# Kernel tuning notes

Measured on AMD Instinct MI355X. Metric: run time of the kernel, lower is better.

Reference implementation:

```python
import jax, jax.numpy as jnp
import numpy as np

M, A, H, T = 6, 4096, 128, 30   # num_modes, num_actors, hidden_size, future_steps
HIST = 50
MAX_T = 6.0
DT = MAX_T / T                   # min_stepsize: one Euler step per prediction interval
MIN_SCALE = 0.001
EPS = 1e-5

def _ln(x, g, b):
    mu = x.mean(-1, keepdims=True)
    v = ((x - mu) ** 2).mean(-1, keepdims=True)
    return (x - mu) * jax.lax.rsqrt(v + EPS) * g + b

def setup_inputs() -> dict:
    key = jax.random.key(0)
    ks = iter(jax.random.split(key, 64))
    def p(shape):
        return jax.random.normal(next(ks), shape, jnp.float32) * 0.02
    inp = {
        'local_embed':  jax.random.normal(next(ks), (A, H), jnp.float32),
        'global_embed': jax.random.normal(next(ks), (M, A, H), jnp.float32),
        'noise':        jax.random.normal(next(ks), (T, M * A, H), jnp.float32),
        # aggr_embed: Linear(2H,H) + LayerNorm
        'aggr_w': p((2 * H, H)), 'aggr_b': p((H,)),
        'aggr_g': jnp.ones((H,), jnp.float32), 'aggr_be': jnp.zeros((H,), jnp.float32),
        # FFunc (posterior drift): Linear(H+2,H)-Tanh-Linear(H,H)-Tanh-Linear(H,H)
        'f_w1': p((H + 2, H)), 'f_b1': p((H,)),
        'f_w2': p((H, H)),     'f_b2': p((H,)),
        'f_w3': p((H, H)),     'f_b3': p((H,)),
        # GFunc (diffusion): Linear(H+2,H)-Tanh-Linear(H,H)-Tanh-Linear(H,1)-Sigmoid
        'g_w1': p((H + 2, H)), 'g_b1': p((H,)),
        'g_w2': p((H, H)),     'g_b2': p((H,)),
        'g_w3': p((H, 1)),     'g_b3': p((1,)),
        # decoder: Linear(H,H)+LN+ReLU+Linear(H,2)
        'd_w1': p((H, H)), 'd_b1': p((H,)),
        'd_g': jnp.ones((H,), jnp.float32), 'd_be': jnp.zeros((H,), jnp.float32),
        'd_w2': p((H, 2)), 'd_b2': p((2,)),
        # scale head (uncertain=True): same structure as decoder
        's_w1': p((H, H)), 's_b1': p((H,)),
        's_g': jnp.ones((H,), jnp.float32), 's_be': jnp.zeros((H,), jnp.float32),
        's_w2': p((H, 2)), 's_b2': p((2,)),
        # pi head: Linear(2H,H)+LN+ReLU+Linear(H,1)
        'p_w1': p((2 * H, H)), 'p_b1': p((H,)),
        'p_g': jnp.ones((H,), jnp.float32), 'p_be': jnp.zeros((H,), jnp.float32),
        'p_w2': p((H, 1)), 'p_b2': p((1,)),
        'padding_mask': jnp.zeros((A, HIST), dtype=bool),
    }
    return inp

def reference(local_embed, global_embed, noise,
              aggr_w, aggr_b, aggr_g, aggr_be,
              f_w1, f_b1, f_w2, f_b2, f_w3, f_b3,
              g_w1, g_b1, g_w2, g_b2, g_w3, g_b3,
              d_w1, d_b1, d_g, d_be, d_w2, d_b2,
              s_w1, s_b1, s_g, s_be, s_w2, s_b2,
              p_w1, p_b1, p_g, p_be, p_w2, p_b2,
              padding_mask):
    N = M * A
    le = jnp.broadcast_to(local_embed, (M, A, H))
    # aggr_embed(cat(global, local))
    x = jnp.concatenate([global_embed, le], axis=-1)
    h0 = jax.nn.relu(_ln(x @ aggr_w + aggr_b, aggr_g, aggr_be)).reshape(N, H)

    def with_time(y, t):
        tc = jnp.ones((y.shape[0], 1), y.dtype) * t
        return jnp.concatenate([y, jnp.sin(tc), jnp.cos(tc)], axis=-1)

    def drift(t, y):  # FFunc
        i = with_time(y, t)
        h = jnp.tanh(i @ f_w1 + f_b1)
        h = jnp.tanh(h @ f_w2 + f_b2)
        return h @ f_w3 + f_b3

    def diffusion(t, y):  # GFunc -> scalar per sample, repeated over dims
        i = with_time(y, t)
        h = jnp.tanh(i @ g_w1 + g_b1)
        h = jnp.tanh(h @ g_w2 + g_b2)
        return jax.nn.sigmoid(h @ g_w3 + g_b3)  # [N,1]

    ts = jnp.linspace(0.0, MAX_T, T + 1)[:-1]  # left endpoints of each Euler step
    sqdt = jnp.sqrt(jnp.asarray(DT, h0.dtype))

    def step(y, tz):
        t, z = tz
        y2 = y + drift(t, y) * DT + diffusion(t, y) * sqdt * z
        return y2, y2

    _, ys = jax.lax.scan(step, h0, (ts, noise))  # [T, N, H]
    sol_y = ys.transpose(1, 0, 2)                # [N, T, H]

    dh = jax.nn.relu(_ln(sol_y @ d_w1 + d_b1, d_g, d_be))
    loc = (dh @ d_w2 + d_b2).reshape(M, A, T, 2)
    sh = jax.nn.relu(_ln(sol_y @ s_w1 + s_b1, s_g, s_be))
    scale = jax.nn.elu(sh @ s_w2 + s_b2) + 1.0 + MIN_SCALE
    scale = scale.reshape(M, A, T, 2)
    loc_out = jnp.concatenate([loc, scale], axis=-1)  # [M, A, T, 4]

    pin = jnp.concatenate([le, global_embed], axis=-1)
    pi = (jax.nn.relu(_ln(pin @ p_w1 + p_b1, p_g, p_be)) @ p_w2 + p_b2)
    pi = pi.squeeze(-1).T                              # [A, M]

    reg_mask = ~padding_mask[:, -T:]
    return loc_out, pi, reg_mask
```

## Files before the change

kernel.cpp:

```cpp
#include <hip/hip_runtime.h>

#define Adim 4096
#define HD 128
#define TSTEPS 30
#define NROWS 24576
#define RBLK 32
#define NBLKS 768
#define DT_C 0.2f
#define SQDT_C 0.44721359549995794f
#define LN_EPS 1e-5f

#define PI_OFF   2949120
#define MASK_OFF 2973696

typedef unsigned short u16;
typedef __bf16 bf16x8 __attribute__((ext_vector_type(8)));
typedef float f32x4 __attribute__((ext_vector_type(4)));

__device__ __forceinline__ u16 f2bf(float x){
    unsigned u = __builtin_bit_cast(unsigned, x);
    u = (u + 0x7fffu + ((u >> 16) & 1u)) >> 16;
    return (u16)u;
}
__device__ __forceinline__ float bf2f(unsigned h){
    unsigned u = (h & 0xffffu) << 16;
    return __builtin_bit_cast(float, u);
}
__device__ __forceinline__ unsigned pack2(float a, float b){
    unsigned r;
    asm("v_cvt_pk_bf16_f32 %0, %1, %2" : "=v"(r) : "v"(a), "v"(b));
    return r;
}
__device__ __forceinline__ float tanh_f(float x){
    return 1.0f - 2.0f / (1.0f + __expf(2.0f * x));
}
__device__ __forceinline__ float sigm_f(float x){
    return 1.0f / (1.0f + __expf(-x));
}
#define SWZ(r,k) ((k) ^ (((r)&7)<<3))

#define MFMA(A,B,C) __builtin_amdgcn_mfma_f32_16x16x32_bf16(A, B, C, 0, 0, 0)

__device__ __forceinline__ void loadW(const u16* __restrict__ img, int lane, int wid,
                                      bf16x8 W[4]) {
    const int c = wid*16 + (lane & 15);
    const int kq = lane >> 4;
#pragma unroll
    for (int kk = 0; kk < 4; ++kk)
        W[kk] = *reinterpret_cast<const bf16x8*>(img + c*HD + SWZ(c, kk*32 + kq*8));
}

__device__ __forceinline__ void gemm1(const u16* __restrict__ act, const bf16x8 (&W)[4],
                                      int lane, f32x4 acc[2]) {
    const int rl = lane & 15, kq = lane >> 4;
#pragma unroll
    for (int tr = 0; tr < 2; ++tr) {
        const int r = tr*16 + rl;
        const u16* arow = act + r*HD;
        f32x4 a = {0.f,0.f,0.f,0.f};
#pragma unroll
        for (int kk = 0; kk < 4; ++kk) {
            bf16x8 bf = *reinterpret_cast<const bf16x8*>(arow + SWZ(r, kk*32 + kq*8));
            a = MFMA(W[kk], bf, a);
        }
        acc[tr] = a;
    }
}
__device__ __forceinline__ void gemm2(const u16* __restrict__ act,
                                      const bf16x8 (&Wx)[4], const bf16x8 (&Wy)[4],
                                      int lane, f32x4 accX[2], f32x4 accY[2]) {
    const int rl = lane & 15, kq = lane >> 4;
#pragma unroll
    for (int tr = 0; tr < 2; ++tr) {
        const int r = tr*16 + rl;
        const u16* arow = act + r*HD;
        f32x4 ax = {0.f,0.f,0.f,0.f}, ay = {0.f,0.f,0.f,0.f};
#pragma unroll
        for (int kk = 0; kk < 4; ++kk) {
            bf16x8 bf = *reinterpret_cast<const bf16x8*>(arow + SWZ(r, kk*32 + kq*8));
            ax = MFMA(Wx[kk], bf, ax);
            ay = MFMA(Wy[kk], bf, ay);
        }
        accX[tr] = ax; accY[tr] = ay;
    }
}
__device__ __forceinline__ void gemm4(const u16* __restrict__ act,
                                      const bf16x8 (&W1)[4], const bf16x8 (&W2)[4],
                                      const bf16x8 (&W3)[4], const bf16x8 (&W4)[4],
                                      int lane, f32x4 a1[2], f32x4 a2[2],
                                      f32x4 a3[2], f32x4 a4[2]) {
    const int rl = lane & 15, kq = lane >> 4;
#pragma unroll
    for (int tr = 0; tr < 2; ++tr) {
        const int r = tr*16 + rl;
        const u16* arow = act + r*HD;
        f32x4 x1={0.f,0.f,0.f,0.f}, x2={0.f,0.f,0.f,0.f};
        f32x4 x3={0.f,0.f,0.f,0.f}, x4={0.f,0.f,0.f,0.f};
#pragma unroll
        for (int kk = 0; kk < 4; ++kk) {
            bf16x8 bf = *reinterpret_cast<const bf16x8*>(arow + SWZ(r, kk*32 + kq*8));
            x1 = MFMA(W1[kk], bf, x1);
            x2 = MFMA(W2[kk], bf, x2);
            x3 = MFMA(W3[kk], bf, x3);
            x4 = MFMA(W4[kk], bf, x4);
        }
        a1[tr]=x1; a2[tr]=x2; a3[tr]=x3; a4[tr]=x4;
    }
}

__device__ __forceinline__ void epiT(const f32x4 acc[2], const float b[4],
                                     u16* dst, int lane, int wid) {
    const int c0 = wid*16 + ((lane>>4)<<2);
    const int rl = lane & 15;
#pragma unroll
    for (int tr = 0; tr < 2; ++tr) {
        int r = tr*16 + rl;
        float v0 = tanh_f(acc[tr][0] + b[0]);
        float v1 = tanh_f(acc[tr][1] + b[1]);
        float v2 = tanh_f(acc[tr][2] + b[2]);
        float v3 = tanh_f(acc[tr][3] + b[3]);
        uint2 pk = { pack2(v0, v1), pack2(v2, v3) };
        *reinterpret_cast<uint2*>(dst + r*HD + SWZ(r, c0)) = pk;
    }
}
__device__ __forceinline__ void epiN(const f32x4 acc[2], const float b[4],
                                     u16* dst, int lane, int wid) {
    const int c0 = wid*16 + ((lane>>4)<<2);
    const int rl = lane & 15;
#pragma unroll
    for (int tr = 0; tr < 2; ++tr) {
        int r = tr*16 + rl;
        uint2 pk = { pack2(acc[tr][0]+b[0], acc[tr][1]+b[1]),
                     pack2(acc[tr][2]+b[2], acc[tr][3]+b[3]) };
        *reinterpret_cast<uint2*>(dst + r*HD + SWZ(r, c0)) = pk;
    }
}
__device__ __forceinline__ void epiF(const f32x4 acc[2], const float* __restrict__ bias,
                                     float* dst, int lane, int wid) {
    const int c0 = wid*16 + ((lane>>4)<<2);
    const int rl = lane & 15;
    float4 b4 = *reinterpret_cast<const float4*>(bias + c0);
#pragma unroll
    for (int tr = 0; tr < 2; ++tr) {
        int r = tr*16 + rl;
        float4 v = { acc[tr][0]+b4.x, acc[tr][1]+b4.y, acc[tr][2]+b4.z, acc[tr][3]+b4.w };
        *reinterpret_cast<float4*>(dst + r*HD + c0) = v;
    }
}

__device__ __forceinline__ void gemmX(const u16* __restrict__ Xc, int kBase,
                                      const u16* __restrict__ img,
                                      int lane, int wid, f32x4 acc[2], bool init) {
    bf16x8 W[4]; loadW(img, lane, wid, W);
    const int rl = lane & 15, kq = lane >> 4;
#pragma unroll
    for (int tr = 0; tr < 2; ++tr) {
        const int r = tr*16 + rl;
        const u16* arow = Xc + r*256;
        f32x4 a = init ? f32x4{0.f,0.f,0.f,0.f} : acc[tr];
#pragma unroll
        for (int kk = 0; kk < 4; ++kk) {
            bf16x8 bf = *reinterpret_cast<const bf16x8*>(arow + SWZ(r, kBase + kk*32 + kq*8));
            a = MFMA(W[kk], bf, a);
        }
        acc[tr] = a;
    }
}

__device__ __forceinline__ void head_ln(const u16* __restrict__ src,
                                        const float4* __restrict__ pp4,
                                        float b20, float b21, int elu, int off, int idx,
                                        float* __restrict__ outStage)
{
    int row = idx >> 3, sub = idx & 7;
    int c0 = sub * 16;
    uint4 p0 = *reinterpret_cast<const uint4*>(src + row*HD + SWZ(row, c0));
    uint4 p1 = *reinterpret_cast<const uint4*>(src + row*HD + SWZ(row, c0+8));
    float v[16];
    v[0]=bf2f(p0.x); v[1]=bf2f(p0.x>>16); v[2]=bf2f(p0.y); v[3]=bf2f(p0.y>>16);
    v[4]=bf2f(p0.z); v[5]=bf2f(p0.z>>16); v[6]=bf2f(p0.w); v[7]=bf2f(p0.w>>16);
    v[8]=bf2f(p1.x); v[9]=bf2f(p1.x>>16); v[10]=bf2f(p1.y); v[11]=bf2f(p1.y>>16);
    v[12]=bf2f(p1.z); v[13]=bf2f(p1.z>>16); v[14]=bf2f(p1.w); v[15]=bf2f(p1.w>>16);
    float s = 0.f, sq = 0.f;
#pragma unroll
    for (int i = 0; i < 16; ++i){ s += v[i]; sq += v[i]*v[i]; }
    s += __shfl_xor(s,1); sq += __shfl_xor(sq,1);
    s += __shfl_xor(s,2); sq += __shfl_xor(sq,2);
    s += __shfl_xor(s,4); sq += __shfl_xor(sq,4);
    float mu = s * (1.f/128.f);
    float rstd = rsqrtf(sq*(1.f/128.f) - mu*mu + LN_EPS);
    float a0 = 0.f, a1 = 0.f;
#pragma unroll
    for (int i = 0; i < 16; ++i){
        float4 p = pp4[(c0 + i) ^ sub];
        float h = (v[i]-mu)*rstd*p.x + p.y;
        h = fmaxf(h, 0.f);
        a0 += h * p.z; a1 += h * p.w;
    }
    a0 += __shfl_xor(a0,1); a1 += __shfl_xor(a1,1);
    a0 += __shfl_xor(a0,2); a1 += __shfl_xor(a1,2);
    a0 += __shfl_xor(a0,4); a1 += __shfl_xor(a1,4);
    if (sub == 0){
        a0 += b20; a1 += b21;
        if (elu){
            a0 = (a0 > 0.f ? a0 : __expf(a0)-1.f) + 1.001f;
            a1 = (a1 > 0.f ? a1 : __expf(a1)-1.f) + 1.001f;
        }
        outStage[row*4 + off]   = a0;
        outStage[row*4 + off+1] = a1;
    }
}

__global__ void prep_w(const float* __restrict__ fw1, const float* __restrict__ fw2,
                       const float* __restrict__ fw3, const float* __restrict__ gw1,
                       const float* __restrict__ gw2, const float* __restrict__ dw1,
                       const float* __restrict__ sw1, const float* __restrict__ aw,
                       const float* __restrict__ pw1, u16* __restrict__ ws)
{
    int img = blockIdx.y;
    int idx = blockIdx.x * 256 + threadIdx.x;
    int k = idx >> 7, j = idx & 127;
    const float* W = fw1; int sr = k;
    switch (img) {
        case 0: W = fw1; break;  case 1: W = fw2; break;  case 2: W = fw3; break;
        case 3: W = gw1; break;  case 4: W = gw2; break;
        case 5: W = dw1; break;  case 6: W = sw1; break;
        case 7: W = aw;  break;  case 8: W = aw;  sr = k + 128; break;
        case 9: W = pw1; break;  case 10: W = pw1; sr = k + 128; break;
    }
    ws[(size_t)img*16384 + j*128 + SWZ(j, k)] = f2bf(W[(size_t)sr*128 + j]);
}

__global__ void reorder_out(const float* __restrict__ wsOut, float* __restrict__ outp)
{
    __shared__ float tile[3840];
    int b = blockIdx.x;
    const float* src = wsOut + (size_t)b*3840;
#pragma unroll
    for (int j = 0; j < 15; ++j) {
        int idx = j*256 + threadIdx.x;
        int tt = idx >> 7, rc = idx & 127;
        int row = rc >> 2, c = idx & 3;
        tile[row*120 + tt*4 + c] = src[idx];
    }
    __syncthreads();
    float* dst = outp + (size_t)b*3840;
#pragma unroll
    for (int j = 0; j < 15; ++j) {
        int idx = j*256 + threadIdx.x;
        dst[idx] = tile[idx];
    }
}

__global__ __launch_bounds__(512, 2) void sde_fused(
    const float* __restrict__ lE, const float* __restrict__ gE,
    const float* __restrict__ noise,
    const float* __restrict__ aggr_b, const float* __restrict__ aggr_g, const float* __restrict__ aggr_be,
    const float* __restrict__ fw1, const float* __restrict__ fb1,
    const float* __restrict__ fb2, const float* __restrict__ fb3,
    const float* __restrict__ gw1, const float* __restrict__ gb1,
    const float* __restrict__ gb2, const float* __restrict__ gw3, const float* __restrict__ gb3,
    const float* __restrict__ db1, const float* __restrict__ dg, const float* __restrict__ dbe,
    const float* __restrict__ dw2, const float* __restrict__ db2,
    const float* __restrict__ sb1, const float* __restrict__ sg, const float* __restrict__ sbe,
    const float* __restrict__ sw2, const float* __restrict__ sb2,
    const float* __restrict__ pb1, const float* __restrict__ pg, const float* __restrict__ pbe,
    const float* __restrict__ pw2, const float* __restrict__ pb2,
    const unsigned char* __restrict__ pmask,
    const u16* __restrict__ wimg,
    float* __restrict__ wsOut,
    float* __restrict__ outp)
{
    __shared__ __align__(16) unsigned char SMEM[61952];
    u16*  Sb    = (u16*)SMEM;
    u16*  Ab    = (u16*)(SMEM + 8192);
    u16*  Bb    = (u16*)(SMEM + 16384);
    u16*  Cb    = (u16*)(SMEM + 24576);
    u16*  Fb    = (u16*)(SMEM + 32768);
    u16*  Db    = (u16*)(SMEM + 40960);
    u16*  Eb    = (u16*)(SMEM + 49152);
    float4* ppd = (float4*)(SMEM + 57344);
    float4* pps = (float4*)(SMEM + 59392);
    float* outStage = (float*)(SMEM + 61440);
    u16*  Xc    = (u16*)(SMEM + 40960);
    float* preLN = (float*)(SMEM + 8192);

    const int tid  = threadIdx.x;
    const int lane = tid & 63;
    const int wid  = tid >> 6;
    const int bid  = blockIdx.x;
    const int r0   = bid * RBLK;
    const int c0e  = wid*16 + ((lane>>4)<<2);

    if (tid < 128) {
        int cs = tid ^ ((tid >> 4) & 7);
        ppd[cs] = make_float4(dg[tid], dbe[tid], dw2[2*tid], dw2[2*tid+1]);
        pps[cs] = make_float4(sg[tid], sbe[tid], sw2[2*tid], sw2[2*tid+1]);
    }
#pragma unroll
    for (int i = 0; i < 2; ++i) {
        int gidx = i*512 + tid;
        int r = gidx >> 5;
        int k = (gidx & 31) * 8;
        int gr = r0 + r;
        const float* src = (k < HD) ? (gE + (size_t)gr*HD + k)
                                    : (lE + (size_t)(gr & (Adim-1))*HD + (k - HD));
        float4 v0 = reinterpret_cast<const float4*>(src)[0];
        float4 v1 = reinterpret_cast<const float4*>(src)[1];
        uint4 pk = { pack2(v0.x, v0.y), pack2(v0.z, v0.w),
                     pack2(v1.x, v1.y), pack2(v1.z, v1.w) };
        *reinterpret_cast<uint4*>(Xc + r*256 + SWZ(r, k)) = pk;
    }
    __syncthreads();

    f32x4 acc[2];

    gemmX(Xc, 0,   wimg + 10*16384, lane, wid, acc, true);
    gemmX(Xc, 128, wimg + 9*16384,  lane, wid, acc, false);
    epiF(acc, pb1, preLN, lane, wid);
    __syncthreads();
    {
        int row = tid >> 4, sub = tid & 15;
        int c0 = sub * 8;
        const float* yr = preLN + row*HD + c0;
        float v[8]; float s = 0.f, sq = 0.f;
#pragma unroll
        for (int i = 0; i < 8; ++i){ float x = yr[i]; v[i] = x; s += x; sq += x*x; }
        s += __shfl_xor(s,1); sq += __shfl_xor(sq,1);
        s += __shfl_xor(s,2); sq += __shfl_xor(sq,2);
        s += __shfl_xor(s,4); sq += __shfl_xor(sq,4);
        s += __shfl_xor(s,8); sq += __shfl_xor(sq,8);
        float mu = s*(1.f/128.f);
        float rstd = rsqrtf(sq*(1.f/128.f) - mu*mu + LN_EPS);
        float a0 = 0.f;
#pragma unroll
        for (int i = 0; i < 8; ++i){
            int cc = c0 + i;
            float h = (v[i]-mu)*rstd*pg[cc] + pbe[cc];
            a0 += fmaxf(h, 0.f) * pw2[cc];
        }
        a0 += __shfl_xor(a0,1); a0 += __shfl_xor(a0,2);
        a0 += __shfl_xor(a0,4); a0 += __shfl_xor(a0,8);
        if (sub == 0) {
            int gr = r0 + row;
            outp[PI_OFF + (size_t)(gr & (Adim-1))*6 + (gr >> 12)] = a0 + pb2[0];
        }
    }
    if (tid < RBLK) {
        int gr = r0 + tid;
        if (gr < Adim) {
            const unsigned char* pm = pmask + (size_t)gr*50 + 20;
            float* o = outp + MASK_OFF + (size_t)gr*TSTEPS;
#pragma unroll
            for (int i = 0; i < TSTEPS; ++i) o[i] = pm[i] ? 0.f : 1.f;
        }
    }
    __syncthreads();

    gemmX(Xc, 0,   wimg + 7*16384, lane, wid, acc, true);
    gemmX(Xc, 128, wimg + 8*16384, lane, wid, acc, false);
    __syncthreads();
    epiF(acc, aggr_b, preLN, lane, wid);
    __syncthreads();

    float y0,y1,y2,y3,y4,y5,y6,y7;
    {
        int row = tid >> 4, sub = tid & 15;
        int c0 = sub * 8;
        const float* yr = preLN + row*HD + c0;
        float v[8]; float s = 0.f, sq = 0.f;
#pragma unroll
        for (int i = 0; i < 8; ++i){ float x = yr[i]; v[i] = x; s += x; sq += x*x; }
        s += __shfl_xor(s,1); sq += __shfl_xor(sq,1);
        s += __shfl_xor(s,2); sq += __shfl_xor(sq,2);
        s += __shfl_xor(s,4); sq += __shfl_xor(sq,4);
        s += __shfl_xor(s,8); sq += __shfl_xor(sq,8);
        float mu = s*(1.f/128.f);
        float rstd = rsqrtf(sq*(1.f/128.f) - mu*mu + LN_EPS);
#pragma unroll
        for (int i = 0; i < 8; ++i){
            int cc = c0 + i;
            float h = (v[i]-mu)*rstd*aggr_g[cc] + aggr_be[cc];
            v[i] = fmaxf(h, 0.f);
        }
        y0=v[0]; y1=v[1]; y2=v[2]; y3=v[3]; y4=v[4]; y5=v[5]; y6=v[6]; y7=v[7];
        uint4 pk = { pack2(v[0],v[1]), pack2(v[2],v[3]),
                     pack2(v[4],v[5]), pack2(v[6],v[7]) };
        *reinterpret_cast<uint4*>(&Sb[row*HD + SWZ(row, c0)]) = pk;
    }

    bf16x8 WF1[4], WG1[4], WF2[4], WG2[4], WF3[4], WD1[4], WS1[4];
    loadW(wimg + 0*16384, lane, wid, WF1);
    loadW(wimg + 3*16384, lane, wid, WG1);
    loadW(wimg + 1*16384, lane, wid, WF2);
    loadW(wimg + 4*16384, lane, wid, WG2);
    loadW(wimg + 2*16384, lane, wid, WF3);
    loadW(wimg + 5*16384, lane, wid, WD1);
    loadW(wimg + 6*16384, lane, wid, WS1);

    float fb2c[4], gb2c[4], fb3c[4], db1c[4], sb1c[4];
    float fb1c[4], gb1c[4], fw1s[4], fw1cc[4], gw1s[4], gw1cc[4];
#pragma unroll
    for (int q = 0; q < 4; ++q) {
        int c = c0e + q;
        fb2c[q]=fb2[c]; gb2c[q]=gb2[c]; fb3c[q]=fb3[c]; db1c[q]=db1[c]; sb1c[q]=sb1[c];
        fb1c[q]=fb1[c]; gb1c[q]=gb1[c];
        fw1s[q]=fw1[128*HD+c]; fw1cc[q]=fw1[129*HD+c];
        gw1s[q]=gw1[128*HD+c]; gw1cc[q]=gw1[129*HD+c];
    }
    float g3r[8];
#pragma unroll
    for (int j = 0; j < 8; ++j) g3r[j] = gw3[(tid & 15)*8 + j];
    const float db20 = db2[0], db21 = db2[1];
    const float sb20 = sb2[0], sb21 = sb2[1];
    const float gb3v = gb3[0];

    float4 nz0, nz1;
    __syncthreads();

    {
        float bF[4], bG[4];
#pragma unroll
        for (int q = 0; q < 4; ++q) { bF[q] = fb1c[q] + fw1cc[q]; bG[q] = gb1c[q] + gw1cc[q]; }
        f32x4 aF[2], aG[2];
        gemm2(Sb, WF1, WG1, lane, aF, aG);
        epiT(aF, bF, Ab, lane, wid);
        epiT(aG, bG, Bb, lane, wid);
        const float* np = noise + ((size_t)r0)*HD + (size_t)tid*8;
        nz0 = reinterpret_cast<const float4*>(np)[0];
        nz1 = reinterpret_cast<const float4*>(np)[1];
    }
    __syncthreads();

    for (int k = 0; k < TSTEPS; ++k) {
        {
            f32x4 a1[2];
            gemm1(Ab, WF2, lane, a1);
            epiT(a1, fb2c, Cb, lane, wid);
            gemm1(Bb, WG2, lane, a1);
            epiT(a1, gb2c, Fb, lane, wid);
        }
        if (k) {
            if (tid < 256) head_ln(Db, ppd, db20, db21, 0, 0, tid, outStage);
            else           head_ln(Eb, pps, sb20, sb21, 1, 2, tid-256, outStage);
        }
        __syncthreads();
        {
            f32x4 a1[2];
            gemm1(Cb, WF3, lane, a1);
            epiN(a1, fb3c, Db, lane, wid);
        }
        float growv;
        {
            int row = tid >> 4, sub = tid & 15;
            uint4 pk = *reinterpret_cast<const uint4*>(Fb + row*HD + SWZ(row, sub*8));
            float s = bf2f(pk.x)*g3r[0] + bf2f(pk.x>>16)*g3r[1]
                    + bf2f(pk.y)*g3r[2] + bf2f(pk.y>>16)*g3r[3]
                    + bf2f(pk.z)*g3r[4] + bf2f(pk.z>>16)*g3r[5]
                    + bf2f(pk.w)*g3r[6] + bf2f(pk.w>>16)*g3r[7];
            s += __shfl_xor(s,1); s += __shfl_xor(s,2);
            s += __shfl_xor(s,4); s += __shfl_xor(s,8);
            growv = sigm_f(s + gb3v);
        }
        __syncthreads();
        {
            int row = tid >> 4, sub = tid & 15;
            int sk = SWZ(row, sub*8);
            uint4 dpk = *reinterpret_cast<const uint4*>(Db + row*HD + sk);
            float g = growv * SQDT_C;
            y0 += bf2f(dpk.x)     * DT_C + g*nz0.x;
            y1 += bf2f(dpk.x>>16) * DT_C + g*nz0.y;
            y2 += bf2f(dpk.y)     * DT_C + g*nz0.z;
            y3 += bf2f(dpk.y>>16) * DT_C + g*nz0.w;
            y4 += bf2f(dpk.z)     * DT_C + g*nz1.x;
            y5 += bf2f(dpk.z>>16) * DT_C + g*nz1.y;
            y6 += bf2f(dpk.w)     * DT_C + g*nz1.z;
            y7 += bf2f(dpk.w>>16) * DT_C + g*nz1.w;
            uint4 s4 = { pack2(y0,y1), pack2(y2,y3), pack2(y4,y5), pack2(y6,y7) };
            *reinterpret_cast<uint4*>(Sb + row*HD + sk) = s4;
        }
        __syncthreads();
        if (k < TSTEPS-1) {
            float t = (k+1) * DT_C;
            float st = __sinf(t), ct = __cosf(t);
            float bF[4], bG[4];
#pragma unroll
            for (int q = 0; q < 4; ++q) {
                bF[q] = fb1c[q] + st*fw1s[q] + ct*fw1cc[q];
                bG[q] = gb1c[q] + st*gw1s[q] + ct*gw1cc[q];
            }
            f32x4 aF[2], aG[2], aD[2], aS[2];
            gemm4(Sb, WF1, WG1, WD1, WS1, lane, aF, aG, aD, aS);
            epiT(aF, bF, Ab, lane, wid);
            epiT(aG, bG, Bb, lane, wid);
            epiN(aD, db1c, Db, lane, wid);
            epiN(aS, sb1c, Eb, lane, wid);
            const float* np = noise + ((size_t)(k+1)*NROWS + r0)*HD + (size_t)tid*8;
            nz0 = reinterpret_cast<const float4*>(np)[0];
            nz1 = reinterpret_cast<const float4*>(np)[1];
            if (k >= 1 && tid < 128)
                wsOut[((size_t)bid*TSTEPS + (k-1))*128 + tid] = outStage[tid];
        } else {
            f32x4 aD[2], aS[2];
            gemm2(Sb, WD1, WS1, lane, aD, aS);
            epiN(aD, db1c, Db, lane, wid);
            epiN(aS, sb1c, Eb, lane, wid);
            if (tid < 128)
                wsOut[((size_t)bid*TSTEPS + (TSTEPS-2))*128 + tid] = outStage[tid];
        }
        __syncthreads();
    }
    if (tid < 256) head_ln(Db, ppd, db20, db21, 0, 0, tid, outStage);
    else           head_ln(Eb, pps, sb20, sb21, 1, 2, tid-256, outStage);
    __syncthreads();
    if (tid < 128)
        wsOut[((size_t)bid*TSTEPS + (TSTEPS-1))*128 + tid] = outStage[tid];
}

extern "C" void kernel_launch(void* const* d_in, const int* in_sizes, int n_in,
                              void* d_out, int out_size, void* d_ws, size_t ws_size,
                              hipStream_t stream) {
    const float* lE      = (const float*)d_in[0];
    const float* gE      = (const float*)d_in[1];
    const float* noise   = (const float*)d_in[2];
    const float* aggr_w  = (const float*)d_in[3];
    const float* aggr_b  = (const float*)d_in[4];
    const float* aggr_g  = (const float*)d_in[5];
    const float* aggr_be = (const float*)d_in[6];
    const float* fw1 = (const float*)d_in[7];
    const float* fb1 = (const float*)d_in[8];
    const float* fw2 = (const float*)d_in[9];
    const float* fb2 = (const float*)d_in[10];
    const float* fw3 = (const float*)d_in[11];
    const float* fb3 = (const float*)d_in[12];
    const float* gw1 = (const float*)d_in[13];
    const float* gb1 = (const float*)d_in[14];
    const float* gw2 = (const float*)d_in[15];
    const float* gb2 = (const float*)d_in[16];
    const float* gw3 = (const float*)d_in[17];
    const float* gb3 = (const float*)d_in[18];
    const float* dw1 = (const float*)d_in[19];
    const float* db1 = (const float*)d_in[20];
    const float* dg  = (const float*)d_in[21];
    const float* dbe = (const float*)d_in[22];
    const float* dw2 = (const float*)d_in[23];
    const float* db2 = (const float*)d_in[24];
    const float* sw1 = (const float*)d_in[25];
    const float* sb1 = (const float*)d_in[26];
    const float* sg  = (const float*)d_in[27];
    const float* sbe = (const float*)d_in[28];
    const float* sw2 = (const float*)d_in[29];
    const float* sb2 = (const float*)d_in[30];
    const float* pw1 = (const float*)d_in[31];
    const float* pb1 = (const float*)d_in[32];
    const float* pg  = (const float*)d_in[33];
    const float* pbe = (const float*)d_in[34];
    const float* pw2 = (const float*)d_in[35];
    const float* pb2 = (const float*)d_in[36];
    const unsigned char* pmask = (const unsigned char*)d_in[37];
    float* outp = (float*)d_out;
    u16* wimg = (u16*)d_ws;
    float* wsOut = (float*)((char*)d_ws + 360448);

    prep_w<<<dim3(64, 11), 256, 0, stream>>>(fw1, fw2, fw3, gw1, gw2, dw1, sw1,
                                             aggr_w, pw1, wimg);
    sde_fused<<<NBLKS, 512, 0, stream>>>(
        lE, gE, noise, aggr_b, aggr_g, aggr_be,
        fw1, fb1, fb2, fb3,
        gw1, gb1, gb2, gw3, gb3,
        db1, dg, dbe, dw2, db2,
        sb1, sg, sbe, sw2, sb2,
        pb1, pg, pbe, pw2, pb2,
        pmask, wimg, wsOut, outp);
    reorder_out<<<NBLKS, 256, 0, stream>>>(wsOut, outp);
}
```

Measured before the change: 593.5 us.

## Enlarge row tile to 48, keep SDE state in registers, restructure step barriers

Raises rows per block from 32 to 48 (512 blocks), so each wave does three 16-row MFMA tiles per loaded weight fragment. The Euler state y moves into MFMA-output-layout registers. The diffusion output projection is fused into the second G-layer epilogue through a small partial-sum buffer, which removes the Fb buffer and one pass. The step loop is reordered so the decoder/scale GEMMs run on the previous state alongside the drift layers, and the head LayerNorm overlaps the state update. Shared memory grows to about 85KB per block, which may limit residency to one block per CU despite launch_bounds(512,2), and 128 threads sit idle in the LN phases.

Result: slower. 912.7 us (+53.8%).

```diff
diff --git a/kernel.cpp b/kernel.cpp
--- a/kernel.cpp
+++ b/kernel.cpp
@@ -4,8 +4,8 @@
 #define HD 128
 #define TSTEPS 30
 #define NROWS 24576
-#define RBLK 32
-#define NBLKS 768
+#define RBLK 48
+#define NBLKS 512
 #define DT_C 0.2f
 #define SQDT_C 0.44721359549995794f
 #define LN_EPS 1e-5f
@@ -38,7 +38,6 @@
     return 1.0f / (1.0f + __expf(-x));
 }
 #define SWZ(r,k) ((k) ^ (((r)&7)<<3))
-
 #define MFMA(A,B,C) __builtin_amdgcn_mfma_f32_16x16x32_bf16(A, B, C, 0, 0, 0)
 
 __device__ __forceinline__ void loadW(const u16* __restrict__ img, int lane, int wid,
@@ -51,10 +50,10 @@
 }
 
 __device__ __forceinline__ void gemm1(const u16* __restrict__ act, const bf16x8 (&W)[4],
-                                      int lane, f32x4 acc[2]) {
+                                      int lane, f32x4 acc[3]) {
     const int rl = lane & 15, kq = lane >> 4;
 #pragma unroll
-    for (int tr = 0; tr < 2; ++tr) {
+    for (int tr = 0; tr < 3; ++tr) {
         const int r = tr*16 + rl;
         const u16* arow = act + r*HD;
         f32x4 a = {0.f,0.f,0.f,0.f};
@@ -68,10 +67,10 @@
 }
 __device__ __forceinline__ void gemm2(const u16* __restrict__ act,
                                       const bf16x8 (&Wx)[4], const bf16x8 (&Wy)[4],
-                                      int lane, f32x4 accX[2], f32x4 accY[2]) {
+                                      int lane, f32x4 accX[3], f32x4 accY[3]) {
     const int rl = lane & 15, kq = lane >> 4;
 #pragma unroll
-    for (int tr = 0; tr < 2; ++tr) {
+    for (int tr = 0; tr < 3; ++tr) {
         const int r = tr*16 + rl;
         const u16* arow = act + r*HD;
         f32x4 ax = {0.f,0.f,0.f,0.f}, ay = {0.f,0.f,0.f,0.f};
@@ -84,36 +83,13 @@
         accX[tr] = ax; accY[tr] = ay;
     }
 }
-__device__ __forceinline__ void gemm4(const u16* __restrict__ act,
-                                      const bf16x8 (&W1)[4], const bf16x8 (&W2)[4],
-                                      const bf16x8 (&W3)[4], const bf16x8 (&W4)[4],
-                                      int lane, f32x4 a1[2], f32x4 a2[2],
-                                      f32x4 a3[2], f32x4 a4[2]) {
-    const int rl = lane & 15, kq = lane >> 4;
-#pragma unroll
-    for (int tr = 0; tr < 2; ++tr) {
-        const int r = tr*16 + rl;
-        const u16* arow = act + r*HD;
-        f32x4 x1={0.f,0.f,0.f,0.f}, x2={0.f,0.f,0.f,0.f};
-        f32x4 x3={0.f,0.f,0.f,0.f}, x4={0.f,0.f,0.f,0.f};
-#pragma unroll
-        for (int kk = 0; kk < 4; ++kk) {
-            bf16x8 bf = *reinterpret_cast<const bf16x8*>(arow + SWZ(r, kk*32 + kq*8));
-            x1 = MFMA(W1[kk], bf, x1);
-            x2 = MFMA(W2[kk], bf, x2);
-            x3 = MFMA(W3[kk], bf, x3);
-            x4 = MFMA(W4[kk], bf, x4);
-        }
-        a1[tr]=x1; a2[tr]=x2; a3[tr]=x3; a4[tr]=x4;
-    }
-}
-
-__device__ __forceinline__ void epiT(const f32x4 acc[2], const float b[4],
+
+__device__ __forceinline__ void epiT(const f32x4 acc[3], const float b[4],
                                      u16* dst, int lane, int wid) {
     const int c0 = wid*16 + ((lane>>4)<<2);
     const int rl = lane & 15;
 #pragma unroll
-    for (int tr = 0; tr < 2; ++tr) {
+    for (int tr = 0; tr < 3; ++tr) {
         int r = tr*16 + rl;
         float v0 = tanh_f(acc[tr][0] + b[0]);
         float v1 = tanh_f(acc[tr][1] + b[1]);
@@ -123,25 +99,25 @@
         *reinterpret_cast<uint2*>(dst + r*HD + SWZ(r, c0)) = pk;
     }
 }
-__device__ __forceinline__ void epiN(const f32x4 acc[2], const float b[4],
+__device__ __forceinline__ void epiN(const f32x4 acc[3], const float b[4],
                                      u16* dst, int lane, int wid) {
     const int c0 = wid*16 + ((lane>>4)<<2);
     const int rl = lane & 15;
 #pragma unroll
-    for (int tr = 0; tr < 2; ++tr) {
+    for (int tr = 0; tr < 3; ++tr) {
         int r = tr*16 + rl;
         uint2 pk = { pack2(acc[tr][0]+b[0], acc[tr][1]+b[1]),
                      pack2(acc[tr][2]+b[2], acc[tr][3]+b[3]) };
         *reinterpret_cast<uint2*>(dst + r*HD + SWZ(r, c0)) = pk;
     }
 }
-__device__ __forceinline__ void epiF(const f32x4 acc[2], const float* __restrict__ bias,
+__device__ __forceinline__ void epiF(const f32x4 acc[3], const float* __restrict__ bias,
                                      float* dst, int lane, int wid) {
     const int c0 = wid*16 + ((lane>>4)<<2);
     const int rl = lane & 15;
     float4 b4 = *reinterpret_cast<const float4*>(bias + c0);
 #pragma unroll
-    for (int tr = 0; tr < 2; ++tr) {
+    for (int tr = 0; tr < 3; ++tr) {
         int r = tr*16 + rl;
         float4 v = { acc[tr][0]+b4.x, acc[tr][1]+b4.y, acc[tr][2]+b4.z, acc[tr][3]+b4.w };
         *reinterpret_cast<float4*>(dst + r*HD + c0) = v;
@@ -150,11 +126,11 @@
 
 __device__ __forceinline__ void gemmX(const u16* __restrict__ Xc, int kBase,
                                       const u16* __restrict__ img,
-                                      int lane, int wid, f32x4 acc[2], bool init) {
+                                      int lane, int wid, f32x4 acc[3], bool init) {
     bf16x8 W[4]; loadW(img, lane, wid, W);
     const int rl = lane & 15, kq = lane >> 4;
 #pragma unroll
-    for (int tr = 0; tr < 2; ++tr) {
+    for (int tr = 0; tr < 3; ++tr) {
         const int r = tr*16 + rl;
         const u16* arow = Xc + r*256;
         f32x4 a = init ? f32x4{0.f,0.f,0.f,0.f} : acc[tr];
@@ -167,40 +143,41 @@
     }
 }
 
-__device__ __forceinline__ void head_ln(const u16* __restrict__ src,
-                                        const float4* __restrict__ pp4,
-                                        float b20, float b21, int elu, int off, int idx,
-                                        float* __restrict__ outStage)
+__device__ __forceinline__ void head_ln4(const u16* __restrict__ src,
+                                         const float4* __restrict__ pp4,
+                                         float b20, float b21, int elu, int off,
+                                         int idx, float* __restrict__ outStage)
 {
-    int row = idx >> 3, sub = idx & 7;
-    int c0 = sub * 16;
-    uint4 p0 = *reinterpret_cast<const uint4*>(src + row*HD + SWZ(row, c0));
-    uint4 p1 = *reinterpret_cast<const uint4*>(src + row*HD + SWZ(row, c0+8));
-    float v[16];
-    v[0]=bf2f(p0.x); v[1]=bf2f(p0.x>>16); v[2]=bf2f(p0.y); v[3]=bf2f(p0.y>>16);
-    v[4]=bf2f(p0.z); v[5]=bf2f(p0.z>>16); v[6]=bf2f(p0.w); v[7]=bf2f(p0.w>>16);
-    v[8]=bf2f(p1.x); v[9]=bf2f(p1.x>>16); v[10]=bf2f(p1.y); v[11]=bf2f(p1.y>>16);
-    v[12]=bf2f(p1.z); v[13]=bf2f(p1.z>>16); v[14]=bf2f(p1.w); v[15]=bf2f(p1.w>>16);
+    int row = idx >> 2, part = idx & 3;
+    int c0 = part * 32;
+    float v[32];
+#pragma unroll
+    for (int u = 0; u < 4; ++u) {
+        uint4 p = *reinterpret_cast<const uint4*>(src + row*HD + SWZ(row, c0 + u*8));
+        v[u*8+0]=bf2f(p.x); v[u*8+1]=bf2f(p.x>>16);
+        v[u*8+2]=bf2f(p.y); v[u*8+3]=bf2f(p.y>>16);
+        v[u*8+4]=bf2f(p.z); v[u*8+5]=bf2f(p.z>>16);
+        v[u*8+6]=bf2f(p.w); v[u*8+7]=bf2f(p.w>>16);
+    }
     float s = 0.f, sq = 0.f;
 #pragma unroll
-    for (int i = 0; i < 16; ++i){ s += v[i]; sq += v[i]*v[i]; }
+    for (int i = 0; i < 32; ++i){ s += v[i]; sq += v[i]*v[i]; }
     s += __shfl_xor(s,1); sq += __shfl_xor(sq,1);
     s += __shfl_xor(s,2); sq += __shfl_xor(sq,2);
-    s += __shfl_xor(s,4); sq += __shfl_xor(sq,4);
     float mu = s * (1.f/128.f);
     float rstd = rsqrtf(sq*(1.f/128.f) - mu*mu + LN_EPS);
     float a0 = 0.f, a1 = 0.f;
 #pragma unroll
-    for (int i = 0; i < 16; ++i){
-        float4 p = pp4[(c0 + i) ^ sub];
+    for (int i = 0; i < 32; ++i){
+        int c = c0 + i;
+        float4 p = pp4[c ^ ((c>>4)&7)];
         float h = (v[i]-mu)*rstd*p.x + p.y;
         h = fmaxf(h, 0.f);
         a0 += h * p.z; a1 += h * p.w;
     }
     a0 += __shfl_xor(a0,1); a1 += __shfl_xor(a1,1);
     a0 += __shfl_xor(a0,2); a1 += __shfl_xor(a1,2);
-    a0 += __shfl_xor(a0,4); a1 += __shfl_xor(a1,4);
-    if (sub == 0){
+    if (part == 0){
         a0 += b20; a1 += b21;
         if (elu){
             a0 = (a0 > 0.f ? a0 : __expf(a0)-1.f) + 1.001f;
@@ -233,23 +210,19 @@
 
 __global__ void reorder_out(const float* __restrict__ wsOut, float* __restrict__ outp)
 {
-    __shared__ float tile[3840];
+    __shared__ float tile[5760];
     int b = blockIdx.x;
-    const float* src = wsOut + (size_t)b*3840;
-#pragma unroll
-    for (int j = 0; j < 15; ++j) {
-        int idx = j*256 + threadIdx.x;
-        int tt = idx >> 7, rc = idx & 127;
-        int row = rc >> 2, c = idx & 3;
-        tile[row*120 + tt*4 + c] = src[idx];
-    }
-    __syncthreads();
-    float* dst = outp + (size_t)b*3840;
-#pragma unroll
-    for (int j = 0; j < 15; ++j) {
-        int idx = j*256 + threadIdx.x;
-        dst[idx] = tile[idx];
-    }
+    int tid = threadIdx.x;
+    const float* src = wsOut + (size_t)b*5760;
+    int row = tid >> 2, c = tid & 3;
+#pragma unroll
+    for (int j = 0; j < TSTEPS; ++j)
+        tile[row*120 + j*4 + c] = src[j*192 + tid];
+    __syncthreads();
+    float* dst = outp + (size_t)b*5760;
+#pragma unroll
+    for (int j = 0; j < TSTEPS; ++j)
+        dst[j*192 + tid] = tile[j*192 + tid];
 }
 
 __global__ __launch_bounds__(512, 2) void sde_fused(
@@ -271,25 +244,26 @@
     float* __restrict__ wsOut,
     float* __restrict__ outp)
 {
-    __shared__ __align__(16) unsigned char SMEM[61952];
+    __shared__ __align__(16) unsigned char SMEM[85120];
     u16*  Sb    = (u16*)SMEM;
-    u16*  Ab    = (u16*)(SMEM + 8192);
-    u16*  Bb    = (u16*)(SMEM + 16384);
-    u16*  Cb    = (u16*)(SMEM + 24576);
-    u16*  Fb    = (u16*)(SMEM + 32768);
-    u16*  Db    = (u16*)(SMEM + 40960);
-    u16*  Eb    = (u16*)(SMEM + 49152);
-    float4* ppd = (float4*)(SMEM + 57344);
-    float4* pps = (float4*)(SMEM + 59392);
-    float* outStage = (float*)(SMEM + 61440);
-    u16*  Xc    = (u16*)(SMEM + 40960);
-    float* preLN = (float*)(SMEM + 8192);
+    u16*  Ab    = (u16*)(SMEM + 12288);
+    u16*  Bb    = (u16*)(SMEM + 24576);
+    u16*  Cb    = (u16*)(SMEM + 36864);
+    u16*  Db    = (u16*)(SMEM + 49152);
+    u16*  Eb    = (u16*)(SMEM + 61440);
+    float* gpart = (float*)(SMEM + 73728);
+    float4* ppd = (float4*)(SMEM + 80256);
+    float4* pps = (float4*)(SMEM + 82304);
+    float* outStage = (float*)(SMEM + 84352);
+    u16*  Xc    = (u16*)(SMEM + 49152);
+    float* preLN = (float*)(SMEM + 12288);
 
     const int tid  = threadIdx.x;
     const int lane = tid & 63;
     const int wid  = tid >> 6;
     const int bid  = blockIdx.x;
     const int r0   = bid * RBLK;
+    const int rl   = lane & 15;
     const int c0e  = wid*16 + ((lane>>4)<<2);
 
     if (tid < 128) {
@@ -298,7 +272,7 @@
         pps[cs] = make_float4(sg[tid], sbe[tid], sw2[2*tid], sw2[2*tid+1]);
     }
 #pragma unroll
-    for (int i = 0; i < 2; ++i) {
+    for (int i = 0; i < 3; ++i) {
         int gidx = i*512 + tid;
         int r = gidx >> 5;
         int k = (gidx & 31) * 8;
@@ -313,34 +287,32 @@
     }
     __syncthreads();
 
-    f32x4 acc[2];
-
-    gemmX(Xc, 0,   wimg + 10*16384, lane, wid, acc, true);
-    gemmX(Xc, 128, wimg + 9*16384,  lane, wid, acc, false);
-    epiF(acc, pb1, preLN, lane, wid);
-    __syncthreads();
-    {
-        int row = tid >> 4, sub = tid & 15;
-        int c0 = sub * 8;
+    f32x4 acc3[3];
+
+    gemmX(Xc, 0,   wimg + 10*16384, lane, wid, acc3, true);
+    gemmX(Xc, 128, wimg + 9*16384,  lane, wid, acc3, false);
+    epiF(acc3, pb1, preLN, lane, wid);
+    __syncthreads();
+    if (tid < 384) {
+        int row = tid >> 3, sub = tid & 7;
+        int c0 = sub * 16;
         const float* yr = preLN + row*HD + c0;
-        float v[8]; float s = 0.f, sq = 0.f;
-#pragma unroll
-        for (int i = 0; i < 8; ++i){ float x = yr[i]; v[i] = x; s += x; sq += x*x; }
+        float v[16]; float s = 0.f, sq = 0.f;
+#pragma unroll
+        for (int i = 0; i < 16; ++i){ float x = yr[i]; v[i] = x; s += x; sq += x*x; }
         s += __shfl_xor(s,1); sq += __shfl_xor(sq,1);
         s += __shfl_xor(s,2); sq += __shfl_xor(sq,2);
         s += __shfl_xor(s,4); sq += __shfl_xor(sq,4);
-        s += __shfl_xor(s,8); sq += __shfl_xor(sq,8);
         float mu = s*(1.f/128.f);
         float rstd = rsqrtf(sq*(1.f/128.f) - mu*mu + LN_EPS);
         float a0 = 0.f;
 #pragma unroll
-        for (int i = 0; i < 8; ++i){
+        for (int i = 0; i < 16; ++i){
             int cc = c0 + i;
             float h = (v[i]-mu)*rstd*pg[cc] + pbe[cc];
             a0 += fmaxf(h, 0.f) * pw2[cc];
         }
-        a0 += __shfl_xor(a0,1); a0 += __shfl_xor(a0,2);
-        a0 += __shfl_xor(a0,4); a0 += __shfl_xor(a0,8);
+        a0 += __shfl_xor(a0,1); a0 += __shfl_xor(a0,2); a0 += __shfl_xor(a0,4);
         if (sub == 0) {
             int gr = r0 + row;
             outp[PI_OFF + (size_t)(gr & (Adim-1))*6 + (gr >> 12)] = a0 + pb2[0];
@@ -357,36 +329,46 @@
     }
     __syncthreads();
 
-    gemmX(Xc, 0,   wimg + 7*16384, lane, wid, acc, true);
-    gemmX(Xc, 128, wimg + 8*16384, lane, wid, acc, false);
-    __syncthreads();
-    epiF(acc, aggr_b, preLN, lane, wid);
-    __syncthreads();
-
-    float y0,y1,y2,y3,y4,y5,y6,y7;
-    {
-        int row = tid >> 4, sub = tid & 15;
-        int c0 = sub * 8;
-        const float* yr = preLN + row*HD + c0;
-        float v[8]; float s = 0.f, sq = 0.f;
-#pragma unroll
-        for (int i = 0; i < 8; ++i){ float x = yr[i]; v[i] = x; s += x; sq += x*x; }
+    gemmX(Xc, 0,   wimg + 7*16384, lane, wid, acc3, true);
+    gemmX(Xc, 128, wimg + 8*16384, lane, wid, acc3, false);
+    __syncthreads();
+    epiF(acc3, aggr_b, preLN, lane, wid);
+    __syncthreads();
+    if (tid < 384) {
+        int row = tid >> 3, sub = tid & 7;
+        int c0 = sub * 16;
+        float* yr = preLN + row*HD + c0;
+        float v[16]; float s = 0.f, sq = 0.f;
+#pragma unroll
+        for (int i = 0; i < 16; ++i){ float x = yr[i]; v[i] = x; s += x; sq += x*x; }
         s += __shfl_xor(s,1); sq += __shfl_xor(sq,1);
         s += __shfl_xor(s,2); sq += __shfl_xor(sq,2);
         s += __shfl_xor(s,4); sq += __shfl_xor(sq,4);
-        s += __shfl_xor(s,8); sq += __shfl_xor(sq,8);
         float mu = s*(1.f/128.f);
         float rstd = rsqrtf(sq*(1.f/128.f) - mu*mu + LN_EPS);
 #pragma unroll
-        for (int i = 0; i < 8; ++i){
+        for (int i = 0; i < 16; ++i){
             int cc = c0 + i;
             float h = (v[i]-mu)*rstd*aggr_g[cc] + aggr_be[cc];
             v[i] = fmaxf(h, 0.f);
         }
-        y0=v[0]; y1=v[1]; y2=v[2]; y3=v[3]; y4=v[4]; y5=v[5]; y6=v[6]; y7=v[7];
-        uint4 pk = { pack2(v[0],v[1]), pack2(v[2],v[3]),
-                     pack2(v[4],v[5]), pack2(v[6],v[7]) };
-        *reinterpret_cast<uint4*>(&Sb[row*HD + SWZ(row, c0)]) = pk;
+#pragma unroll
+        for (int u = 0; u < 4; ++u)
+            *reinterpret_cast<float4*>(yr + u*4) = *(float4*)&v[u*4];
+        uint4 pk0 = { pack2(v[0],v[1]), pack2(v[2],v[3]),
+                      pack2(v[4],v[5]), pack2(v[6],v[7]) };
+        uint4 pk1 = { pack2(v[8],v[9]), pack2(v[10],v[11]),
+                      pack2(v[12],v[13]), pack2(v[14],v[15]) };
+        *reinterpret_cast<uint4*>(&Sb[row*HD + SWZ(row, c0)])   = pk0;
+        *reinterpret_cast<uint4*>(&Sb[row*HD + SWZ(row, c0+8)]) = pk1;
+    }
+    __syncthreads();
+
+    float y[12];
+#pragma unroll
+    for (int tr = 0; tr < 3; ++tr) {
+        float4 t = *reinterpret_cast<const float4*>(preLN + (tr*16+rl)*HD + c0e);
+        y[tr*4+0]=t.x; y[tr*4+1]=t.y; y[tr*4+2]=t.z; y[tr*4+3]=t.w;
     }
 
     bf16x8 WF1[4], WG1[4], WF2[4], WG2[4], WF3[4], WD1[4], WS1[4];
@@ -398,90 +380,25 @@
     loadW(wimg + 5*16384, lane, wid, WD1);
     loadW(wimg + 6*16384, lane, wid, WS1);
 
-    float fb2c[4], gb2c[4], fb3c[4], db1c[4], sb1c[4];
+    float fb2c[4], gb2c[4], fb3c[4], db1c[4], sb1c[4], gw3c[4];
     float fb1c[4], gb1c[4], fw1s[4], fw1cc[4], gw1s[4], gw1cc[4];
 #pragma unroll
     for (int q = 0; q < 4; ++q) {
         int c = c0e + q;
         fb2c[q]=fb2[c]; gb2c[q]=gb2[c]; fb3c[q]=fb3[c]; db1c[q]=db1[c]; sb1c[q]=sb1[c];
-        fb1c[q]=fb1[c]; gb1c[q]=gb1[c];
+        fb1c[q]=fb1[c]; gb1c[q]=gb1[c]; gw3c[q]=gw3[c];
         fw1s[q]=fw1[128*HD+c]; fw1cc[q]=fw1[129*HD+c];
         gw1s[q]=gw1[128*HD+c]; gw1cc[q]=gw1[129*HD+c];
     }
-    float g3r[8];
-#pragma unroll
-    for (int j = 0; j < 8; ++j) g3r[j] = gw3[(tid & 15)*8 + j];
     const float db20 = db2[0], db21 = db2[1];
     const float sb20 = sb2[0], sb21 = sb2[1];
     const float gb3v = gb3[0];
-
-    float4 nz0, nz1;
-    __syncthreads();
-
-    {
-        float bF[4], bG[4];
-#pragma unroll
-        for (int q = 0; q < 4; ++q) { bF[q] = fb1c[q] + fw1cc[q]; bG[q] = gb1c[q] + gw1cc[q]; }
-        f32x4 aF[2], aG[2];
-        gemm2(Sb, WF1, WG1, lane, aF, aG);
-        epiT(aF, bF, Ab, lane, wid);
-        epiT(aG, bG, Bb, lane, wid);
-        const float* np = noise + ((size_t)r0)*HD + (size_t)tid*8;
-        nz0 = reinterpret_cast<const float4*>(np)[0];
-        nz1 = reinterpret_cast<const float4*>(np)[1];
-    }
-    __syncthreads();
-
+    __syncthreads();
+
+    float4 nz[3];
     for (int k = 0; k < TSTEPS; ++k) {
         {
-            f32x4 a1[2];
-            gemm1(Ab, WF2, lane, a1);
-            epiT(a1, fb2c, Cb, lane, wid);
-            gemm1(Bb, WG2, lane, a1);
-            epiT(a1, gb2c, Fb, lane, wid);
-        }
-        if (k) {
-            if (tid < 256) head_ln(Db, ppd, db20, db21, 0, 0, tid, outStage);
-            else           head_ln(Eb, pps, sb20, sb21, 1, 2, tid-256, outStage);
-        }
-        __syncthreads();
-        {
-            f32x4 a1[2];
-            gemm1(Cb, WF3, lane, a1);
-            epiN(a1, fb3c, Db, lane, wid);
-        }
-        float growv;
-        {
-            int row = tid >> 4, sub = tid & 15;
-            uint4 pk = *reinterpret_cast<const uint4*>(Fb + row*HD + SWZ(row, sub*8));
-            float s = bf2f(pk.x)*g3r[0] + bf2f(pk.x>>16)*g3r[1]
-                    + bf2f(pk.y)*g3r[2] + bf2f(pk.y>>16)*g3r[3]
-                    + bf2f(pk.z)*g3r[4] + bf2f(pk.z>>16)*g3r[5]
-                    + bf2f(pk.w)*g3r[6] + bf2f(pk.w>>16)*g3r[7];
-            s += __shfl_xor(s,1); s += __shfl_xor(s,2);
-            s += __shfl_xor(s,4); s += __shfl_xor(s,8);
-            growv = sigm_f(s + gb3v);
-        }
-        __syncthreads();
-        {
-            int row = tid >> 4, sub = tid & 15;
-            int sk = SWZ(row, sub*8);
-            uint4 dpk = *reinterpret_cast<const uint4*>(Db + row*HD + sk);
-            float g = growv * SQDT_C;
-            y0 += bf2f(dpk.x)     * DT_C + g*nz0.x;
-            y1 += bf2f(dpk.x>>16) * DT_C + g*nz0.y;
-            y2 += bf2f(dpk.y)     * DT_C + g*nz0.z;
-            y3 += bf2f(dpk.y>>16) * DT_C + g*nz0.w;
-            y4 += bf2f(dpk.z)     * DT_C + g*nz1.x;
-            y5 += bf2f(dpk.z>>16) * DT_C + g*nz1.y;
-            y6 += bf2f(dpk.w)     * DT_C + g*nz1.z;
-            y7 += bf2f(dpk.w>>16) * DT_C + g*nz1.w;
-            uint4 s4 = { pack2(y0,y1), pack2(y2,y3), pack2(y4,y5), pack2(y6,y7) };
-            *reinterpret_cast<uint4*>(Sb + row*HD + sk) = s4;
-        }
-        __syncthreads();
-        if (k < TSTEPS-1) {
-            float t = (k+1) * DT_C;
+            float t = k * DT_C;
             float st = __sinf(t), ct = __cosf(t);
             float bF[4], bG[4];
 #pragma unroll
@@ -489,32 +406,91 @@
                 bF[q] = fb1c[q] + st*fw1s[q] + ct*fw1cc[q];
                 bG[q] = gb1c[q] + st*gw1s[q] + ct*gw1cc[q];
             }
-            f32x4 aF[2], aG[2], aD[2], aS[2];
-            gemm4(Sb, WF1, WG1, WD1, WS1, lane, aF, aG, aD, aS);
+            f32x4 aF[3], aG[3];
+            gemm2(Sb, WF1, WG1, lane, aF, aG);
             epiT(aF, bF, Ab, lane, wid);
             epiT(aG, bG, Bb, lane, wid);
-            epiN(aD, db1c, Db, lane, wid);
-            epiN(aS, sb1c, Eb, lane, wid);
-            const float* np = noise + ((size_t)(k+1)*NROWS + r0)*HD + (size_t)tid*8;
-            nz0 = reinterpret_cast<const float4*>(np)[0];
-            nz1 = reinterpret_cast<const float4*>(np)[1];
-            if (k >= 1 && tid < 128)
-                wsOut[((size_t)bid*TSTEPS + (k-1))*128 + tid] = outStage[tid];
-        } else {
-            f32x4 aD[2], aS[2];
+        }
+#pragma unroll
+        for (int tr = 0; tr < 3; ++tr)
+            nz[tr] = *reinterpret_cast<const float4*>(
+                noise + ((size_t)k*NROWS + r0 + tr*16 + rl)*HD + c0e);
+        if (k >= 2 && tid < 192)
+            wsOut[((size_t)bid*TSTEPS + (k-2))*192 + tid] = outStage[tid];
+        __syncthreads();
+
+        {
+            f32x4 a1[3];
+            gemm1(Ab, WF2, lane, a1);
+            epiT(a1, fb2c, Cb, lane, wid);
+            gemm1(Bb, WG2, lane, a1);
+            const int kq = lane >> 4;
+#pragma unroll
+            for (int tr = 0; tr < 3; ++tr) {
+                float p = tanh_f(a1[tr][0]+gb2c[0]) * gw3c[0]
+                        + tanh_f(a1[tr][1]+gb2c[1]) * gw3c[1]
+                        + tanh_f(a1[tr][2]+gb2c[2]) * gw3c[2]
+                        + tanh_f(a1[tr][3]+gb2c[3]) * gw3c[3];
+                gpart[(tr*16+rl)*34 + wid*4 + kq] = p;
+            }
+        }
+        if (k >= 1) {
+            f32x4 aD[3], aS[3];
             gemm2(Sb, WD1, WS1, lane, aD, aS);
             epiN(aD, db1c, Db, lane, wid);
             epiN(aS, sb1c, Eb, lane, wid);
-            if (tid < 128)
-                wsOut[((size_t)bid*TSTEPS + (TSTEPS-2))*128 + tid] = outStage[tid];
         }
         __syncthreads();
-    }
-    if (tid < 256) head_ln(Db, ppd, db20, db21, 0, 0, tid, outStage);
-    else           head_ln(Eb, pps, sb20, sb21, 1, 2, tid-256, outStage);
-    __syncthreads();
-    if (tid < 128)
-        wsOut[((size_t)bid*TSTEPS + (TSTEPS-1))*128 + tid] = outStage[tid];
+
+        {
+            f32x4 aD3[3];
+            gemm1(Cb, WF3, lane, aD3);
+            const int kq = lane >> 4;
+            float g[3];
+#pragma unroll
+            for (int tr = 0; tr < 3; ++tr) {
+                const float* gp = gpart + (tr*16+rl)*34 + kq*8;
+                float2 u0 = *reinterpret_cast<const float2*>(gp);
+                float2 u1 = *reinterpret_cast<const float2*>(gp+2);
+                float2 u2 = *reinterpret_cast<const float2*>(gp+4);
+                float2 u3 = *reinterpret_cast<const float2*>(gp+6);
+                float s = u0.x+u0.y+u1.x+u1.y+u2.x+u2.y+u3.x+u3.y;
+                s += __shfl_xor(s, 16);
+                s += __shfl_xor(s, 32);
+                g[tr] = sigm_f(s + gb3v) * SQDT_C;
+            }
+#pragma unroll
+            for (int tr = 0; tr < 3; ++tr) {
+                int row = tr*16 + rl;
+                y[tr*4+0] += (aD3[tr][0]+fb3c[0])*DT_C + g[tr]*nz[tr].x;
+                y[tr*4+1] += (aD3[tr][1]+fb3c[1])*DT_C + g[tr]*nz[tr].y;
+                y[tr*4+2] += (aD3[tr][2]+fb3c[2])*DT_C + g[tr]*nz[tr].z;
+                y[tr*4+3] += (aD3[tr][3]+fb3c[3])*DT_C + g[tr]*nz[tr].w;
+                uint2 pk = { pack2(y[tr*4+0],y[tr*4+1]), pack2(y[tr*4+2],y[tr*4+3]) };
+                *reinterpret_cast<uint2*>(Sb + row*HD + SWZ(row, c0e)) = pk;
+            }
+        }
+        if (k >= 1) {
+            if (tid < 192)      head_ln4(Db, ppd, db20, db21, 0, 0, tid, outStage);
+            else if (tid < 384) head_ln4(Eb, pps, sb20, sb21, 1, 2, tid-192, outStage);
+        }
+        __syncthreads();
+    }
+
+    if (tid < 192)
+        wsOut[((size_t)bid*TSTEPS + (TSTEPS-2))*192 + tid] = outStage[tid];
+    {
+        f32x4 aD[3], aS[3];
+        gemm2(Sb, WD1, WS1, lane, aD, aS);
+        epiN(aD, db1c, Db, lane, wid);
+        epiN(aS, sb1c, Eb, lane, wid);
+    }
+    __syncthreads();
+    if (tid < 192)      head_ln4(Db, ppd, db20, db21, 0, 0, tid, outStage);
+    else if (tid < 384) head_ln4(Eb, pps, sb20, sb21, 1, 2, tid-192, outStage);
+    __syncthreads();
+    if (tid < 192)
+        wsOut[((size_t)bid*TSTEPS + (TSTEPS-1))*192 + tid] = outStage[tid];
 }
 
 extern "C" void kernel_launch(void* const* d_in, const int* in_sizes, int n_in,
@@ -572,5 +548,5 @@
         sb1, sg, sbe, sw2, sb2,
         pb1, pg, pbe, pw2, pb2,
         pmask, wimg, wsOut, outp);
-    reorder_out<<<NBLKS, 256, 0, stream>>>(wsOut, outp);
-}
+    reorder_out<<<NBLKS, 192, 0, stream>>>(wsOut, outp);
+}
```
